# Kernel optimization log

Measured on AMD Instinct MI355X. Metric: run time of the kernel, lower is better.

## Reference

```python
import jax, jax.numpy as jnp
import numpy as np

N = 100000       # nodes
E = 1600000      # edges per graph
D_IN, D_H, D_OUT = 256, 64, 32
TEM = (0.9, 0.8)  # tem[0], tem[1]


def setup_inputs() -> dict:
    key = jax.random.key(0)
    ks = jax.random.split(key, 17)
    f32 = jnp.float32
    return {
        "features": jax.random.normal(ks[0], (N, D_IN), f32),
        # GraphConv layer1: glorot-ish weight [in, out] + bias
        "W1": jax.random.normal(ks[1], (D_IN, D_H), f32) / np.sqrt(D_IN).astype(np.float32),
        "b1": jnp.zeros((D_H,), f32),
        "W2": jax.random.normal(ks[2], (D_H, D_OUT), f32) / np.sqrt(D_H).astype(np.float32),
        "b2": jnp.zeros((D_OUT,), f32),
        # gating linears: nn.Linear(2*d, 1) -> weight [1, 2*d], bias [1]
        "ga11_w": jax.random.normal(ks[3], (1, 2 * D_H), f32) * 0.1,
        "ga11_b": jnp.zeros((1,), f32),
        "ga12_w": jax.random.normal(ks[4], (1, 2 * D_H), f32) * 0.1,
        "ga12_b": jnp.zeros((1,), f32),
        "ga21_w": jax.random.normal(ks[5], (1, 2 * D_OUT), f32) * 0.1,
        "ga21_b": jnp.zeros((1,), f32),
        "ga22_w": jax.random.normal(ks[6], (1, 2 * D_OUT), f32) * 0.1,
        "ga22_b": jnp.zeros((1,), f32),
        # two graphs as edge lists over the same N nodes
        "src1": jax.random.randint(ks[7], (E,), 0, N, jnp.int32),
        "dst1": jax.random.randint(ks[8], (E,), 0, N, jnp.int32),
        "src2": jax.random.randint(ks[9], (E,), 0, N, jnp.int32),
        "dst2": jax.random.randint(ks[10], (E,), 0, N, jnp.int32),
    }


def _graph_conv(feat, W, b, src, dst):
    """DGL GraphConv, norm='both': D_dst^{-1/2} A^T D_src^{-1/2} X W + b.
    in_feats > out_feats for both layers, so W is applied before aggregation."""
    ones = jnp.ones(src.shape[0], feat.dtype)
    deg_out = jnp.clip(jax.ops.segment_sum(ones, src, num_segments=N), 1.0)  # [N]
    deg_in = jnp.clip(jax.ops.segment_sum(ones, dst, num_segments=N), 1.0)   # [N]
    h = (feat * jax.lax.rsqrt(deg_out)[:, None]) @ W                          # [N, d_out]
    agg = jax.ops.segment_sum(h[src], dst, num_segments=N)                    # SpMM scatter-add
    return agg * jax.lax.rsqrt(deg_in)[:, None] + b


def _gate(xa, xb, w, b, tem):
    """Faithful to: ga = softmax(Linear(cat[xa,xb]), dim=1); diag(ga) -> ga[0,0];
    xb' = tem * diag * xb. softmax over a size-1 axis gives ones; dropout is a
    no-op in eval mode."""
    ga = jnp.concatenate([xa, xb], axis=1) @ w.T + b  # [N, 1]
    ga = jax.nn.softmax(ga, axis=1)                   # all ones ([N,1], axis of size 1)
    d = ga[0, 0]                                      # torch.diag of [N,1] -> scalar ga[0,0]
    return tem * d * xb


def reference(features, W1, b1, W2, b2, ga11_w, ga11_b, ga12_w, ga12_b,
              ga21_w, ga21_b, ga22_w, ga22_b, src1, dst1, src2, dst2):
    x11 = _graph_conv(features, W1, b1, src1, dst1)
    x12 = _graph_conv(features, W1, b1, src2, dst2)
    x12 = _gate(x11, x12, ga11_w, ga11_b, TEM[1])
    x11 = _gate(x12, x11, ga12_w, ga12_b, TEM[0])
    x1 = x11 + x12
    x21 = _graph_conv(x1, W2, b2, src1, dst1)
    x22 = _graph_conv(x1, W2, b2, src2, dst2)
    x22 = _gate(x21, x22, ga21_w, ga21_b, TEM[1])
    x21 = _gate(x22, x21, ga22_w, ga22_b, TEM[0])
    return x21 + x22
```

## Files before the change

### kernel.cpp

```cpp
#include <hip/hip_runtime.h>
#include <hip/hip_bf16.h>

#define TEM0 0.9f
#define TEM1 0.8f
#define NPB 256
#define CAP 4608
#define CHUNKE 2048
#define MAXBUCK 512

typedef __attribute__((ext_vector_type(8))) short bf16x8;
typedef __attribute__((ext_vector_type(4))) float f32x4;

static __device__ __forceinline__ short f2bf(float x) {
  union { __hip_bfloat16 h; short s; } u;
  u.h = __float2bfloat16(x);
  return u.s;
}
static __device__ __forceinline__ float bf2f(short s) {
  union { float f; unsigned u; } v;
  v.u = ((unsigned)(unsigned short)s) << 16;
  return v.f;
}

__global__ __launch_bounds__(256) void bucket_gemm(
    const int* __restrict__ src1, const int* __restrict__ dst1,
    const int* __restrict__ src2, const int* __restrict__ dst2,
    int* gcur_d, int* gcur_s,
    int* __restrict__ rawD1, int* __restrict__ rawD2,
    unsigned char* __restrict__ rawS1, unsigned char* __restrict__ rawS2,
    int E, int NCH, int NBUCK,
    const float* __restrict__ X, const short* __restrict__ Wb,
    short* __restrict__ Yb, int n)
{
  __shared__ int outR[CHUNKE];
  __shared__ short tick[CHUNKE];
  __shared__ short bkt[CHUNKE];
  __shared__ int hist[MAXBUCK], strt[MAXBUCK], basz[MAXBUCK];
  __shared__ int wsum[4];

  if ((int)blockIdx.x < 2 * NCH) {
    int g = 0, cb = blockIdx.x;
    if (cb >= NCH) { g = 1; cb -= NCH; }
    const int* src = g ? src2 : src1;
    const int* dst = g ? dst2 : dst1;
    int* rawD = g ? rawD2 : rawD1;
    unsigned char* rawS = g ? rawS2 : rawS1;
    int* curD = gcur_d + g * NBUCK;
    int* curS = gcur_s + g * NBUCK;
    int tid = threadIdx.x;
    int lane = tid & 63, wave = tid >> 6;
    int e0 = cb * CHUNKE;
    int K = min(CHUNKE, E - e0);

    hist[tid] = 0; hist[tid + 256] = 0;
    __syncthreads();
    for (int i = tid; i < K; i += 256)
      tick[i] = (short)atomicAdd(&hist[dst[e0 + i] >> 8], 1);
    __syncthreads();
    {
      int h0 = hist[2 * tid], h1 = hist[2 * tid + 1];
      int hs = h0 + h1, v = hs;
#pragma unroll
      for (int off = 1; off < 64; off <<= 1) {
        int t = __shfl_up(v, off);
        if (lane >= off) v += t;
      }
      if (lane == 63) wsum[wave] = v;
      __syncthreads();
      int wpre = 0;
#pragma unroll
      for (int w0 = 0; w0 < 4; ++w0) wpre += (w0 < wave) ? wsum[w0] : 0;
      int excl = wpre + v - hs;
      strt[2 * tid] = excl; strt[2 * tid + 1] = excl + h0;
      for (int b = tid; b < NBUCK; b += 256) {
        int c = hist[b];
        basz[b] = c ? atomicAdd(&curD[b], c) : 0;
      }
    }
    __syncthreads();
    for (int i = tid; i < K; i += 256) {
      int d = dst[e0 + i], s = src[e0 + i];
      int b = d >> 8;
      int q = strt[b] + tick[i];
      outR[q] = ((d & 255) << 17) | s;
      bkt[q] = (short)b;
    }
    __syncthreads();
    for (int i = tid; i < K; i += 256) {
      int b = bkt[i];
      int off = basz[b] + (i - strt[b]);
      if (off < CAP) rawD[(size_t)b * CAP + off] = outR[i];
    }
    __syncthreads();

    hist[tid] = 0; hist[tid + 256] = 0;
    __syncthreads();
    for (int i = tid; i < K; i += 256)
      tick[i] = (short)atomicAdd(&hist[src[e0 + i] >> 8], 1);
    __syncthreads();
    {
      int h0 = hist[2 * tid], h1 = hist[2 * tid + 1];
      int hs = h0 + h1, v = hs;
#pragma unroll
      for (int off = 1; off < 64; off <<= 1) {
        int t = __shfl_up(v, off);
        if (lane >= off) v += t;
      }
      if (lane == 63) wsum[wave] = v;
      __syncthreads();
      int wpre = 0;
#pragma unroll
      for (int w0 = 0; w0 < 4; ++w0) wpre += (w0 < wave) ? wsum[w0] : 0;
      int excl = wpre + v - hs;
      strt[2 * tid] = excl; strt[2 * tid + 1] = excl + h0;
      for (int b = tid; b < NBUCK; b += 256) {
        int c = hist[b];
        basz[b] = c ? atomicAdd(&curS[b], c) : 0;
      }
    }
    __syncthreads();
    unsigned char* outS = (unsigned char*)outR;
    for (int i = tid; i < K; i += 256) {
      int s = src[e0 + i];
      int b = s >> 8;
      int q = strt[b] + tick[i];
      outS[q] = (unsigned char)(s & 255);
      bkt[q] = (short)b;
    }
    __syncthreads();
    for (int i = tid; i < K; i += 256) {
      int b = bkt[i];
      int off = basz[b] + (i - strt[b]);
      if (off < CAP) rawS[(size_t)b * CAP + off] = outS[i];
    }
  } else {
    int bid = (int)blockIdx.x - 2 * NCH;
    int w = threadIdx.x >> 6;
    int l = threadIdx.x & 63;
    int row = bid * 64 + w * 16 + (l & 15);
    int rowc = row < n ? row : n - 1;
    int ko = (l >> 4) << 3;

    f32x4 acc[4] = {};
    const float* xrow = X + (size_t)rowc * 256;

#pragma unroll
    for (int kk = 0; kk < 8; ++kk) {
      const float4* p = reinterpret_cast<const float4*>(xrow + kk * 32 + ko);
      float4 a0 = p[0], a1 = p[1];
      bf16x8 af;
      af[0] = f2bf(a0.x); af[1] = f2bf(a0.y); af[2] = f2bf(a0.z); af[3] = f2bf(a0.w);
      af[4] = f2bf(a1.x); af[5] = f2bf(a1.y); af[6] = f2bf(a1.z); af[7] = f2bf(a1.w);
#pragma unroll
      for (int ct = 0; ct < 4; ++ct) {
        bf16x8 bfrag = *reinterpret_cast<const bf16x8*>(Wb + ((size_t)(ct * 8 + kk) * 64 + l) * 8);
        acc[ct] = __builtin_amdgcn_mfma_f32_16x16x32_bf16(af, bfrag, acc[ct], 0, 0, 0);
      }
    }

    int r0 = bid * 64 + w * 16 + ((l >> 4) << 2);
    int c0 = l & 15;
#pragma unroll
    for (int ct = 0; ct < 4; ++ct) {
#pragma unroll
      for (int i = 0; i < 4; ++i) {
        int r = r0 + i;
        if (r < n) Yb[(size_t)r * 64 + ct * 16 + c0] = f2bf(acc[ct][i]);
      }
    }
  }
}

__global__ __launch_bounds__(256) void hist_src(
    const int* __restrict__ gcur_s,
    const unsigned char* __restrict__ rawS1, const unsigned char* __restrict__ rawS2,
    int* __restrict__ co1, int* __restrict__ co2, int NBUCK, int N)
{
  __shared__ int hist[NPB];
  int g = 0, b = blockIdx.x;
  if (b >= NBUCK) { g = 1; b -= NBUCK; }
  const unsigned char* raw = (g ? rawS2 : rawS1) + (size_t)b * CAP;
  int* co = g ? co2 : co1;
  int K = gcur_s[g * NBUCK + b]; if (K > CAP) K = CAP;
  int tid = threadIdx.x;
  hist[tid] = 0;
  __syncthreads();
  for (int j = tid; j < K; j += 256) atomicAdd(&hist[raw[j]], 1);
  __syncthreads();
  int node = b * NPB + tid;
  if (node < N) co[node] = hist[tid];
}

__global__ __launch_bounds__(256) void sort_dst(
    const int* __restrict__ gcur_d,
    const int* __restrict__ rawD1, const int* __restrict__ rawD2,
    int2* __restrict__ edata1, int2* __restrict__ edata2,
    const int* __restrict__ co1, const int* __restrict__ co2,
    int* __restrict__ ci1, int* __restrict__ ci2,
    int* __restrict__ ns1, int* __restrict__ ns2, int NBUCK, int N)
{
  __shared__ int hist[NPB], strt[NPB];
  __shared__ short tick[CAP];
  __shared__ int sl[CAP];
  __shared__ int wsum[4];
  int g = 0, b = blockIdx.x;
  if (b >= NBUCK) { g = 1; b -= NBUCK; }
  const int* raw = (g ? rawD2 : rawD1) + (size_t)b * CAP;
  int2* edata = g ? edata2 : edata1;
  const int* co = g ? co2 : co1;
  const float tem = g ? TEM1 : TEM0;
  int* ci = g ? ci2 : ci1;
  int* ns = g ? ns2 : ns1;
  int K = gcur_d[g * NBUCK + b]; if (K > CAP) K = CAP;
  int tid = threadIdx.x;
  int lane = tid & 63, wave = tid >> 6;

  hist[tid] = 0;
  __syncthreads();
  for (int j = tid; j < K; j += 256)
    tick[j] = (short)atomicAdd(&hist[raw[j] >> 17], 1);
  __syncthreads();
  int h = hist[tid], v = h;
#pragma unroll
  for (int off = 1; off < 64; off <<= 1) {
    int t = __shfl_up(v, off);
    if (lane >= off) v += t;
  }
  if (lane == 63) wsum[wave] = v;
  __syncthreads();
  int wpre = 0;
#pragma unroll
  for (int w0 = 0; w0 < 4; ++w0) wpre += (w0 < wave) ? wsum[w0] : 0;
  strt[tid] = wpre + v - h;
  __syncthreads();
  for (int j = tid; j < K; j += 256) {
    int r = raw[j];
    sl[strt[r >> 17] + tick[j]] = r & 0x1FFFF;
  }
  __syncthreads();
  size_t gbase = (size_t)b * CAP;
  for (int j = tid; j < K; j += 256) {
    int s = sl[j];
    float c = tem * rsqrtf((float)co[s]);
    edata[gbase + j] = make_int2(s, __float_as_int(c));
  }
  int node = b * NPB + tid;
  if (node < N) { ci[node] = hist[tid]; ns[node] = (int)gbase + strt[tid]; }
}

__global__ __launch_bounds__(256) void prep_w1(
    const float* __restrict__ W, short* __restrict__ Wb)
{
  int t = blockIdx.x * 256 + threadIdx.x;
  if (t >= 2048) return;
  int lane = t & 63;
  int kk = (t >> 6) & 7;
  int ct = t >> 9;
  int col = ct * 16 + (lane & 15);
  int k0 = kk * 32 + ((lane >> 4) << 3);
#pragma unroll
  for (int i = 0; i < 8; ++i)
    Wb[(size_t)t * 8 + i] = f2bf(W[(size_t)(k0 + i) * 64 + col]);
}

template<int DIN, int DOUT, int R>
__global__ __launch_bounds__(256) void gemm_rm_bf(
    const float* __restrict__ X, const float* __restrict__ W,
    short* __restrict__ Yb, int n)
{
  __shared__ float Wl[DIN * DOUT];
  for (int i = threadIdx.x; i < DIN * DOUT; i += 256) Wl[i] = W[i];
  __syncthreads();

  const int col = threadIdx.x % DOUT;
  const int rg  = threadIdx.x / DOUT;
  const int rows_per_block = (256 / DOUT) * R;
  const int row0 = blockIdx.x * rows_per_block + rg * R;

  float acc[R];
#pragma unroll
  for (int r = 0; r < R; ++r) acc[r] = 0.f;

  const float4* X4 = reinterpret_cast<const float4*>(X);

  if (row0 + R <= n) {
    for (int k4 = 0; k4 < DIN / 4; ++k4) {
      float w0 = Wl[(4 * k4 + 0) * DOUT + col];
      float w1 = Wl[(4 * k4 + 1) * DOUT + col];
      float w2 = Wl[(4 * k4 + 2) * DOUT + col];
      float w3 = Wl[(4 * k4 + 3) * DOUT + col];
#pragma unroll
      for (int r = 0; r < R; ++r) {
        float4 x = X4[(size_t)(row0 + r) * (DIN / 4) + k4];
        acc[r] = fmaf(x.x, w0, fmaf(x.y, w1, fmaf(x.z, w2, fmaf(x.w, w3, acc[r]))));
      }
    }
#pragma unroll
    for (int r = 0; r < R; ++r)
      Yb[(size_t)(row0 + r) * DOUT + col] = f2bf(acc[r]);
  } else {
    for (int k4 = 0; k4 < DIN / 4; ++k4) {
      float w0 = Wl[(4 * k4 + 0) * DOUT + col];
      float w1 = Wl[(4 * k4 + 1) * DOUT + col];
      float w2 = Wl[(4 * k4 + 2) * DOUT + col];
      float w3 = Wl[(4 * k4 + 3) * DOUT + col];
#pragma unroll
      for (int r = 0; r < R; ++r) {
        if (row0 + r < n) {
          float4 x = X4[(size_t)(row0 + r) * (DIN / 4) + k4];
          acc[r] = fmaf(x.x, w0, fmaf(x.y, w1, fmaf(x.z, w2, fmaf(x.w, w3, acc[r]))));
        }
      }
    }
    for (int r = 0; r < R; ++r)
      if (row0 + r < n) Yb[(size_t)(row0 + r) * DOUT + col] = f2bf(acc[r]);
  }
}

template<int D>
__global__ __launch_bounds__(256) void gather_nodes_bf(
    const int* __restrict__ ci1, const int* __restrict__ ns1, const int2* __restrict__ edata1,
    const int* __restrict__ ci2, const int* __restrict__ ns2, const int2* __restrict__ edata2,
    const short* __restrict__ Yb, const float* __restrict__ bias,
    float bscale, float* __restrict__ out, int n)
{
  constexpr int LPR = D / 8;
  constexpr int EPI = 64 / LPR;
  int wid  = (blockIdx.x * 256 + threadIdx.x) >> 6;
  int lane = threadIdx.x & 63;
  int grp = lane / LPR;
  int li  = lane % LPR;
  if (wid >= n) return;

  const bf16x8* Y8 = reinterpret_cast<const bf16x8*>(Yb);
  float a1[8], a2[8];
#pragma unroll
  for (int k = 0; k < 8; ++k) { a1[k] = 0.f; a2[k] = 0.f; }

  int len1 = ci1[wid], st1 = ns1[wid];
  int len2 = ci2[wid], st2 = ns2[wid];
  int lmax = len1 > len2 ? len1 : len2;

  for (int j = grp; j < lmax; j += EPI) {
    bool p1 = j < len1, p2 = j < len2;
    int2 e1 = p1 ? edata1[st1 + j] : make_int2(0, 0);
    int2 e2 = p2 ? edata2[st2 + j] : make_int2(0, 0);
    float c1 = __int_as_float(e1.y);
    float c2 = __int_as_float(e2.y);
    bf16x8 v1 = Y8[(size_t)e1.x * LPR + li];
    bf16x8 v2 = Y8[(size_t)e2.x * LPR + li];
#pragma unroll
    for (int k = 0; k < 8; ++k) {
      a1[k] = fmaf(c1, bf2f(v1[k]), a1[k]);
      a2[k] = fmaf(c2, bf2f(v2[k]), a2[k]);
    }
  }

  float r1 = rsqrtf((float)(len1 < 1 ? 1 : len1));
  float r2 = rsqrtf((float)(len2 < 1 ? 1 : len2));
  float acc[8];
#pragma unroll
  for (int k = 0; k < 8; ++k) acc[k] = fmaf(r1, a1[k], r2 * a2[k]);

#pragma unroll
  for (int m = LPR; m < 64; m <<= 1) {
#pragma unroll
    for (int k = 0; k < 8; ++k) acc[k] += __shfl_xor(acc[k], m);
  }

  if (grp == 0) {
    float4 b0 = reinterpret_cast<const float4*>(bias)[li * 2];
    float4 b1v = reinterpret_cast<const float4*>(bias)[li * 2 + 1];
    float4 o0, o1;
    o0.x = fmaf(bscale, b0.x, acc[0]);
    o0.y = fmaf(bscale, b0.y, acc[1]);
    o0.z = fmaf(bscale, b0.z, acc[2]);
    o0.w = fmaf(bscale, b0.w, acc[3]);
    o1.x = fmaf(bscale, b1v.x, acc[4]);
    o1.y = fmaf(bscale, b1v.y, acc[5]);
    o1.z = fmaf(bscale, b1v.z, acc[6]);
    o1.w = fmaf(bscale, b1v.w, acc[7]);
    float4* op = reinterpret_cast<float4*>(out + (size_t)wid * D + li * 8);
    op[0] = o0;
    op[1] = o1;
  }
}

extern "C" void kernel_launch(void* const* d_in, const int* in_sizes, int n_in,
                              void* d_out, int out_size, void* d_ws, size_t ws_size,
                              hipStream_t stream)
{
  const float* features = (const float*)d_in[0];
  const float* W1 = (const float*)d_in[1];
  const float* b1 = (const float*)d_in[2];
  const float* W2 = (const float*)d_in[3];
  const float* b2 = (const float*)d_in[4];
  const int* src1 = (const int*)d_in[13];
  const int* dst1 = (const int*)d_in[14];
  const int* src2 = (const int*)d_in[15];
  const int* dst2 = (const int*)d_in[16];

  const int N = in_sizes[0] / 256;
  const int E = in_sizes[13];
  const int NBUCK = (N + NPB - 1) / NPB;
  const int NCH = (E + CHUNKE - 1) / CHUNKE;

  char* ws = (char*)d_ws;
  int* gcur_d = (int*)ws;
  int* gcur_s = gcur_d + 2 * NBUCK;
  int* rawD1  = gcur_s + 2 * NBUCK;
  int* rawD2  = rawD1 + (size_t)NBUCK * CAP;
  unsigned char* rawS1 = (unsigned char*)(rawD2 + (size_t)NBUCK * CAP);
  unsigned char* rawS2 = rawS1 + (size_t)NBUCK * CAP;
  int2* edata1 = (int2*)(rawS2 + (size_t)NBUCK * CAP);
  int2* edata2 = edata1 + (size_t)NBUCK * CAP;
  int* ci1 = (int*)(edata2 + (size_t)NBUCK * CAP);
  int* ci2 = ci1 + N;
  int* ns1 = ci2 + N;
  int* ns2 = ns1 + N;
  int* co1 = ns2 + N;
  int* co2 = co1 + N;
  short* Yb  = (short*)(co2 + N);
  short* Y2b = Yb + (size_t)N * 64;
  short* Wb  = Y2b + (size_t)N * 32;
  float* x1  = (float*)(Wb + 16384);
  float* out = (float*)d_out;

  (void)hipMemsetAsync(gcur_d, 0, (size_t)4 * NBUCK * sizeof(int), stream);
  prep_w1<<<8, 256, 0, stream>>>(W1, Wb);

  const int nbGemm = (N + 63) / 64;
  bucket_gemm<<<2 * NCH + nbGemm, 256, 0, stream>>>(
      src1, dst1, src2, dst2, gcur_d, gcur_s,
      rawD1, rawD2, rawS1, rawS2, E, NCH, NBUCK,
      features, Wb, Yb, N);

  hist_src<<<2 * NBUCK, 256, 0, stream>>>(gcur_s, rawS1, rawS2, co1, co2, NBUCK, N);
  sort_dst<<<2 * NBUCK, 256, 0, stream>>>(gcur_d, rawD1, rawD2, edata1, edata2,
                                          co1, co2, ci1, ci2, ns1, ns2, NBUCK, N);

  gather_nodes_bf<64><<<(N + 3) / 4, 256, 0, stream>>>(
      ci1, ns1, edata1, ci2, ns2, edata2, Yb, b1, TEM0 + TEM1, x1, N);

  gemm_rm_bf<64, 32, 8><<<(N + 63) / 64, 256, 0, stream>>>(x1, W2, Y2b, N);
  gather_nodes_bf<32><<<(N + 3) / 4, 256, 0, stream>>>(
      ci1, ns1, edata1, ci2, ns2, edata2, Y2b, b2, TEM0 + TEM1, out, N);
}
```

Measured before the change: 307.0 us.

## Pack edge data to 32 bits, fuse dst/src bucketing, interleave bucket and GEMM blocks

Edge records become a single 32-bit word holding a 17-bit source index and a 15-bit bf16 coefficient with the sign bit dropped. This halves the edge-stream bytes read by the gather kernels and written by sort_dst. The bucketing kernel now builds the dst and src histograms, scans and scatters in one pass instead of two sequential passes, which cuts barriers and index reloads at the cost of more shared memory. Bucketing blocks and GEMM blocks are interleaved in the grid so both kinds of work share the GPU concurrently. The coefficient is rounded to bf16, which loses precision, and the smaller record only works while node indices fit in 17 bits.

```diff
diff --git a/kernel.cpp b/kernel.cpp
--- a/kernel.cpp
+++ b/kernel.cpp
@@ -33,13 +33,27 @@
     short* __restrict__ Yb, int n)
 {
   __shared__ int outR[CHUNKE];
-  __shared__ short tick[CHUNKE];
-  __shared__ short bkt[CHUNKE];
-  __shared__ int hist[MAXBUCK], strt[MAXBUCK], basz[MAXBUCK];
-  __shared__ int wsum[4];
-
-  if ((int)blockIdx.x < 2 * NCH) {
-    int g = 0, cb = blockIdx.x;
+  __shared__ unsigned char outS[CHUNKE];
+  __shared__ unsigned short tickD[CHUNKE];
+  __shared__ unsigned short tickS[CHUNKE];
+  __shared__ short bktD[CHUNKE];
+  __shared__ short bktS[CHUNKE];
+  __shared__ int histD[MAXBUCK], histS[MAXBUCK];
+  __shared__ int strtD[MAXBUCK], strtS[MAXBUCK];
+  __shared__ int baszD[MAXBUCK], baszS[MAXBUCK];
+  __shared__ int wsumD[4], wsumS[4];
+
+  const int nbB = 2 * NCH;
+  const int nbG = (n + 63) / 64;
+  const int half = nbB < nbG ? nbB : nbG;
+  int bi = (int)blockIdx.x;
+  bool isB;
+  int bid;
+  if (bi < 2 * half) { isB = ((bi & 1) == 0); bid = bi >> 1; }
+  else               { isB = (nbB > nbG);     bid = bi - half; }
+
+  if (isB) {
+    int g = 0, cb = bid;
     if (cb >= NCH) { g = 1; cb -= NCH; }
     const int* src = g ? src2 : src1;
     const int* dst = g ? dst2 : dst1;
@@ -52,89 +66,72 @@
     int e0 = cb * CHUNKE;
     int K = min(CHUNKE, E - e0);
 
-    hist[tid] = 0; hist[tid + 256] = 0;
+    histD[tid] = 0; histD[tid + 256] = 0;
+    histS[tid] = 0; histS[tid + 256] = 0;
     __syncthreads();
-    for (int i = tid; i < K; i += 256)
-      tick[i] = (short)atomicAdd(&hist[dst[e0 + i] >> 8], 1);
-    __syncthreads();
-    {
-      int h0 = hist[2 * tid], h1 = hist[2 * tid + 1];
-      int hs = h0 + h1, v = hs;
-#pragma unroll
-      for (int off = 1; off < 64; off <<= 1) {
-        int t = __shfl_up(v, off);
-        if (lane >= off) v += t;
-      }
-      if (lane == 63) wsum[wave] = v;
-      __syncthreads();
-      int wpre = 0;
-#pragma unroll
-      for (int w0 = 0; w0 < 4; ++w0) wpre += (w0 < wave) ? wsum[w0] : 0;
-      int excl = wpre + v - hs;
-      strt[2 * tid] = excl; strt[2 * tid + 1] = excl + h0;
-      for (int b = tid; b < NBUCK; b += 256) {
-        int c = hist[b];
-        basz[b] = c ? atomicAdd(&curD[b], c) : 0;
-      }
-    }
-    __syncthreads();
+
     for (int i = tid; i < K; i += 256) {
       int d = dst[e0 + i], s = src[e0 + i];
-      int b = d >> 8;
-      int q = strt[b] + tick[i];
-      outR[q] = ((d & 255) << 17) | s;
-      bkt[q] = (short)b;
+      tickD[i] = (unsigned short)atomicAdd(&histD[d >> 8], 1);
+      tickS[i] = (unsigned short)atomicAdd(&histS[s >> 8], 1);
     }
     __syncthreads();
+
+    {
+      int d0 = histD[2 * tid], d1 = histD[2 * tid + 1];
+      int s0 = histS[2 * tid], s1 = histS[2 * tid + 1];
+      int dv = d0 + d1, sv = s0 + s1;
+      int vd = dv, vs = sv;
+#pragma unroll
+      for (int off = 1; off < 64; off <<= 1) {
+        int td = __shfl_up(vd, off);
+        int ts = __shfl_up(vs, off);
+        if (lane >= off) { vd += td; vs += ts; }
+      }
+      if (lane == 63) { wsumD[wave] = vd; wsumS[wave] = vs; }
+      __syncthreads();
+      int wpD = 0, wpS = 0;
+#pragma unroll
+      for (int w0 = 0; w0 < 4; ++w0) {
+        wpD += (w0 < wave) ? wsumD[w0] : 0;
+        wpS += (w0 < wave) ? wsumS[w0] : 0;
+      }
+      int exD = wpD + vd - dv;
+      int exS = wpS + vs - sv;
+      strtD[2 * tid] = exD; strtD[2 * tid + 1] = exD + d0;
+      strtS[2 * tid] = exS; strtS[2 * tid + 1] = exS + s0;
+      for (int b = tid; b < NBUCK; b += 256) {
+        int c = histD[b];
+        baszD[b] = c ? atomicAdd(&curD[b], c) : 0;
+        c = histS[b];
+        baszS[b] = c ? atomicAdd(&curS[b], c) : 0;
+      }
+    }
+    __syncthreads();
+
     for (int i = tid; i < K; i += 256) {
-      int b = bkt[i];
-      int off = basz[b] + (i - strt[b]);
+      int d = dst[e0 + i], s = src[e0 + i];
+      int bD = d >> 8, bS = s >> 8;
+      int qD = strtD[bD] + (int)tickD[i];
+      int qS = strtS[bS] + (int)tickS[i];
+      outR[qD] = ((d & 255) << 17) | s;
+      bktD[qD] = (short)bD;
+      outS[qS] = (unsigned char)(s & 255);
+      bktS[qS] = (short)bS;
+    }
+    __syncthreads();
+
+    for (int i = tid; i < K; i += 256) {
+      int b = bktD[i];
+      int off = baszD[b] + (i - strtD[b]);
       if (off < CAP) rawD[(size_t)b * CAP + off] = outR[i];
     }
-    __syncthreads();
-
-    hist[tid] = 0; hist[tid + 256] = 0;
-    __syncthreads();
-    for (int i = tid; i < K; i += 256)
-      tick[i] = (short)atomicAdd(&hist[src[e0 + i] >> 8], 1);
-    __syncthreads();
-    {
-      int h0 = hist[2 * tid], h1 = hist[2 * tid + 1];
-      int hs = h0 + h1, v = hs;
-#pragma unroll
-      for (int off = 1; off < 64; off <<= 1) {
-        int t = __shfl_up(v, off);
-        if (lane >= off) v += t;
-      }
-      if (lane == 63) wsum[wave] = v;
-      __syncthreads();
-      int wpre = 0;
-#pragma unroll
-      for (int w0 = 0; w0 < 4; ++w0) wpre += (w0 < wave) ? wsum[w0] : 0;
-      int excl = wpre + v - hs;
-      strt[2 * tid] = excl; strt[2 * tid + 1] = excl + h0;
-      for (int b = tid; b < NBUCK; b += 256) {
-        int c = hist[b];
-        basz[b] = c ? atomicAdd(&curS[b], c) : 0;
-      }
-    }
-    __syncthreads();
-    unsigned char* outS = (unsigned char*)outR;
     for (int i = tid; i < K; i += 256) {
-      int s = src[e0 + i];
-      int b = s >> 8;
-      int q = strt[b] + tick[i];
-      outS[q] = (unsigned char)(s & 255);
-      bkt[q] = (short)b;
-    }
-    __syncthreads();
-    for (int i = tid; i < K; i += 256) {
-      int b = bkt[i];
-      int off = basz[b] + (i - strt[b]);
+      int b = bktS[i];
+      int off = baszS[b] + (i - strtS[b]);
       if (off < CAP) rawS[(size_t)b * CAP + off] = outS[i];
     }
   } else {
-    int bid = (int)blockIdx.x - 2 * NCH;
     int w = threadIdx.x >> 6;
     int l = threadIdx.x & 63;
     int row = bid * 64 + w * 16 + (l & 15);
@@ -194,7 +191,7 @@
 __global__ __launch_bounds__(256) void sort_dst(
     const int* __restrict__ gcur_d,
     const int* __restrict__ rawD1, const int* __restrict__ rawD2,
-    int2* __restrict__ edata1, int2* __restrict__ edata2,
+    unsigned* __restrict__ edata1, unsigned* __restrict__ edata2,
     const int* __restrict__ co1, const int* __restrict__ co2,
     int* __restrict__ ci1, int* __restrict__ ci2,
     int* __restrict__ ns1, int* __restrict__ ns2, int NBUCK, int N)
@@ -206,7 +203,7 @@
   int g = 0, b = blockIdx.x;
   if (b >= NBUCK) { g = 1; b -= NBUCK; }
   const int* raw = (g ? rawD2 : rawD1) + (size_t)b * CAP;
-  int2* edata = g ? edata2 : edata1;
+  unsigned* edata = g ? edata2 : edata1;
   const int* co = g ? co2 : co1;
   const float tem = g ? TEM1 : TEM0;
   int* ci = g ? ci2 : ci1;
@@ -242,7 +239,8 @@
   for (int j = tid; j < K; j += 256) {
     int s = sl[j];
     float c = tem * rsqrtf((float)co[s]);
-    edata[gbase + j] = make_int2(s, __float_as_int(c));
+    unsigned cb = (unsigned)(unsigned short)f2bf(c) & 0x7FFFu;
+    edata[gbase + j] = (cb << 17) | (unsigned)s;
   }
   int node = b * NPB + tid;
   if (node < N) { ci[node] = hist[tid]; ns[node] = (int)gbase + strt[tid]; }
@@ -319,8 +317,8 @@
 
 template<int D>
 __global__ __launch_bounds__(256) void gather_nodes_bf(
-    const int* __restrict__ ci1, const int* __restrict__ ns1, const int2* __restrict__ edata1,
-    const int* __restrict__ ci2, const int* __restrict__ ns2, const int2* __restrict__ edata2,
+    const int* __restrict__ ci1, const int* __restrict__ ns1, const unsigned* __restrict__ edata1,
+    const int* __restrict__ ci2, const int* __restrict__ ns2, const unsigned* __restrict__ edata2,
     const short* __restrict__ Yb, const float* __restrict__ bias,
     float bscale, float* __restrict__ out, int n)
 {
@@ -343,12 +341,14 @@
 
   for (int j = grp; j < lmax; j += EPI) {
     bool p1 = j < len1, p2 = j < len2;
-    int2 e1 = p1 ? edata1[st1 + j] : make_int2(0, 0);
-    int2 e2 = p2 ? edata2[st2 + j] : make_int2(0, 0);
-    float c1 = __int_as_float(e1.y);
-    float c2 = __int_as_float(e2.y);
-    bf16x8 v1 = Y8[(size_t)e1.x * LPR + li];
-    bf16x8 v2 = Y8[(size_t)e2.x * LPR + li];
+    unsigned u1 = p1 ? edata1[st1 + j] : 0u;
+    unsigned u2 = p2 ? edata2[st2 + j] : 0u;
+    float c1 = __uint_as_float((u1 >> 17) << 16);
+    float c2 = __uint_as_float((u2 >> 17) << 16);
+    int s1 = (int)(u1 & 0x1FFFFu);
+    int s2 = (int)(u2 & 0x1FFFFu);
+    bf16x8 v1 = Y8[(size_t)s1 * LPR + li];
+    bf16x8 v2 = Y8[(size_t)s2 * LPR + li];
 #pragma unroll
     for (int k = 0; k < 8; ++k) {
       a1[k] = fmaf(c1, bf2f(v1[k]), a1[k]);
@@ -412,8 +412,8 @@
   int* rawD2  = rawD1 + (size_t)NBUCK * CAP;
   unsigned char* rawS1 = (unsigned char*)(rawD2 + (size_t)NBUCK * CAP);
   unsigned char* rawS2 = rawS1 + (size_t)NBUCK * CAP;
-  int2* edata1 = (int2*)(rawS2 + (size_t)NBUCK * CAP);
-  int2* edata2 = edata1 + (size_t)NBUCK * CAP;
+  unsigned* edata1 = (unsigned*)(rawS2 + (size_t)NBUCK * CAP);
+  unsigned* edata2 = edata1 + (size_t)NBUCK * CAP;
   int* ci1 = (int*)(edata2 + (size_t)NBUCK * CAP);
   int* ci2 = ci1 + N;
   int* ns1 = ci2 + N;
```

Result: faster. 291.2 us (-5.2%).
